# Performance work log

Hardware: AMD Instinct MI355X
Metric: run time of the kernel (lower is better)

The kernel has to match this reference:

```python
import jax, jax.numpy as jnp
import numpy as np

B, N, E, T, DIN, H, G, ND, NT, L = 4, 10000, 320000, 16, 16, 64, 64, 16, 3, 7


def _mlp2(x, W1, b1, W2, b2):
    # Linear -> LeakyReLU -> (Dropout: eval identity) -> Linear -> LeakyReLU
    h = jax.nn.leaky_relu(x @ W1 + b1)
    return jax.nn.leaky_relu(h @ W2 + b2)


def _gcn_conv(x, src, dst, ew, nt, W1, b1, W2, b2):
    # x: [B,N,D], nt: [B,N,ND], ew: [*,E,1] broadcastable over batch
    x_in = _mlp2(jnp.concatenate([x, nt], axis=-1), W1, b1, W2, b2)  # [B,N,G]
    msgs = x_in[:, src, :] * ew                                      # gather + weight, [B,E,G]
    aggr = jnp.zeros(x_in.shape, x_in.dtype).at[:, dst, :].add(msgs) # scatter-add, [B,N,G]
    return x + aggr


def _gru(x, Wx, Wh, bx, bh):
    # PyTorch-style GRU over time axis. x: [B,N,T,DIN] -> hs: [T,B,N,H]
    xw = jnp.einsum('bntd,dh->tbnh', x, Wx) + bx  # precompute input projections [T,B,N,3H]
    h0 = jnp.zeros(x.shape[:2] + (Wh.shape[0],), x.dtype)

    def step(h, xw_t):
        hw = h @ Wh + bh
        xr, xz, xn = jnp.split(xw_t, 3, axis=-1)
        hr, hz, hn = jnp.split(hw, 3, axis=-1)
        r = jax.nn.sigmoid(xr + hr)
        z = jax.nn.sigmoid(xz + hz)
        n = jnp.tanh(xn + r * hn)
        h_new = (1 - z) * n + z * h
        return h_new, h_new

    _, hs = jax.lax.scan(step, h0, xw)
    return hs


def reference(input_day, edge_attr, gru_Wx, gru_Wh, gru_bx, gru_bh,
              rnn_fc_W, rnn_fc_b,
              e_emb, e_c0_W1, e_c0_b1, e_c0_W2, e_c0_b2,
              e_c1_W1, e_c1_b1, e_c1_W2, e_c1_b2,
              e_fm_W1, e_fm_b1, e_fm_W2, e_fm_b2,
              g_emb, g_c0_W1, g_c0_b1, g_c0_W2, g_c0_b2,
              g_c1_W1, g_c1_b1, g_c1_W2, g_c1_b2,
              gcn_fc_W, gcn_fc_b,
              edge_index, node_type_ids):
    src, dst = edge_index[0], edge_index[1]

    # KRNN encoder (GRU) + max over time + FC head
    hs = _gru(input_day, gru_Wx, gru_Wh, gru_bx, gru_bh)  # [T,B,N,H]
    rnn_out = hs.max(axis=0)                              # kr_out.max(dim=-2) -> [B,N,H]
    y_rnn = rnn_out @ rnn_fc_W + rnn_fc_b                 # [B,N,L]

    # EdgeNet: GCN stack on static edge_attr, then per-edge pair MLP -> gate
    nt_e = jnp.broadcast_to(e_emb[node_type_ids][None], (B, N, ND))
    ew0 = edge_attr.reshape(1, E, 1)
    x = rnn_out
    x = _gcn_conv(x, src, dst, ew0, nt_e, e_c0_W1, e_c0_b1, e_c0_W2, e_c0_b2)
    x = _gcn_conv(x, src, dst, ew0, nt_e, e_c1_W1, e_c1_b1, e_c1_W2, e_c1_b2)
    edge_x = jnp.concatenate([x[:, src, :], x[:, dst, :]], axis=-1)  # [B,E,2G]
    h = jax.nn.leaky_relu(edge_x @ e_fm_W1 + e_fm_b1)
    edge_gate = jax.nn.relu(h @ e_fm_W2 + e_fm_b2)                   # [B,E,1]

    # Main GCNNet with learned edge gates
    nt_g = jnp.broadcast_to(g_emb[node_type_ids][None], (B, N, ND))
    x = rnn_out
    x = _gcn_conv(x, src, dst, edge_gate, nt_g, g_c0_W1, g_c0_b1, g_c0_W2, g_c0_b2)
    x = _gcn_conv(x, src, dst, edge_gate, nt_g, g_c1_W1, g_c1_b1, g_c1_W2, g_c1_b2)
    y_gcn = x @ gcn_fc_W + gcn_fc_b                                  # [B,N,L]

    return y_rnn + y_gcn


def setup_inputs() -> dict:
    key = jax.random.key(0)
    ks = iter(jax.random.split(key, 48))

    def nrm(shape, s=0.1):
        return jax.random.normal(next(ks), shape, jnp.float32) * s

    inp = {}
    inp['input_day'] = jax.random.normal(next(ks), (B, N, T, DIN), jnp.float32)
    inp['edge_index'] = jax.random.randint(next(ks), (2, E), 0, N)
    inp['node_type_ids'] = jax.random.randint(next(ks), (N,), 0, NT)
    inp['edge_attr'] = jax.random.uniform(next(ks), (E,), jnp.float32)

    inp['gru_Wx'] = nrm((DIN, 3 * H))
    inp['gru_Wh'] = nrm((H, 3 * H))
    inp['gru_bx'] = jnp.zeros((3 * H,), jnp.float32)
    inp['gru_bh'] = jnp.zeros((3 * H,), jnp.float32)
    inp['rnn_fc_W'] = nrm((H, L))
    inp['rnn_fc_b'] = jnp.zeros((L,), jnp.float32)

    inp['e_emb'] = nrm((NT, ND))
    inp['g_emb'] = nrm((NT, ND))
    for pre, in_dim in (('e_c0', H + ND), ('e_c1', G + ND), ('g_c0', H + ND), ('g_c1', G + ND)):
        inp[pre + '_W1'] = nrm((in_dim, G))
        inp[pre + '_b1'] = jnp.zeros((G,), jnp.float32)
        inp[pre + '_W2'] = nrm((G, G))
        inp[pre + '_b2'] = jnp.zeros((G,), jnp.float32)

    inp['e_fm_W1'] = nrm((2 * G, G))
    inp['e_fm_b1'] = jnp.zeros((G,), jnp.float32)
    inp['e_fm_W2'] = nrm((G, 1))
    inp['e_fm_b2'] = jnp.zeros((1,), jnp.float32)

    inp['gcn_fc_W'] = nrm((G, L))
    inp['gcn_fc_b'] = jnp.zeros((L,), jnp.float32)
    return inp
```

## Files before the change

### kernel.cpp

```cpp
#include <hip/hip_runtime.h>
#include <hip/hip_bf16.h>

#define NB 4
#define NN 10000
#define NE 320000
#define BN 40000
#define NL 7

typedef float f32x4 __attribute__((ext_vector_type(4)));
typedef __bf16 bf16x8 __attribute__((ext_vector_type(8)));

__device__ __forceinline__ float bf2f(unsigned short u){
  unsigned x = ((unsigned)u) << 16;
  return __builtin_bit_cast(float, x);
}
__device__ __forceinline__ unsigned short f2bf(float f){
  unsigned u = __builtin_bit_cast(unsigned, f);
  u += 0x7fffu + ((u >> 16) & 1u);
  return (unsigned short)(u >> 16);
}
__device__ __forceinline__ bf16x8 zero8(){
  uint4 z = make_uint4(0u,0u,0u,0u);
  return __builtin_bit_cast(bf16x8, z);
}
__device__ __forceinline__ bf16x8 one8(){
  uint4 z = make_uint4(0x3f80u,0u,0u,0u);
  return __builtin_bit_cast(bf16x8, z);
}
__device__ __forceinline__ bf16x8 ld8bf(const unsigned short* p){
  uint4 u = *(const uint4*)p;
  return __builtin_bit_cast(bf16x8, u);
}
__device__ __forceinline__ unsigned pk2(float lo, float hi){
  unsigned r;
  asm("v_cvt_pk_bf16_f32 %0, %1, %2" : "=v"(r) : "v"(lo), "v"(hi));
  return r;
}
__device__ __forceinline__ bf16x8 ld8f(const float* p){
  float4 a = *(const float4*)p;
  float4 b = *(const float4*)(p+4);
  uint4 u = make_uint4(pk2(a.x,a.y), pk2(a.z,a.w), pk2(b.x,b.y), pk2(b.z,b.w));
  return __builtin_bit_cast(bf16x8, u);
}
__device__ __forceinline__ float frcp(float x){ return __builtin_amdgcn_rcpf(x); }
__device__ __forceinline__ float tanh_(float x){ return 1.f - 2.f*frcp(__expf(2.f*x)+1.f); }
__device__ __forceinline__ float lrelu(float x){ return x > 0.f ? x : 0.01f*x; }

#define LDS_WAIT() asm volatile("s_waitcnt lgkmcnt(0)" ::: "memory")

__global__ __launch_bounds__(256, 2) void gru_kernel(
    const float* __restrict__ xd,
    const float* __restrict__ Wx,
    const float* __restrict__ Wh,
    const float* __restrict__ bx,
    const float* __restrict__ bh,
    float* __restrict__ rnn)
{
  __shared__ __attribute__((aligned(16))) unsigned short WhT[192][72];
  __shared__ __attribute__((aligned(16))) unsigned short WxT[192][40];
  __shared__ __attribute__((aligned(16))) unsigned short hb[4][16][76];
  int tid = threadIdx.x;
  int wave = tid >> 6, lane = tid & 63;
  int ln16 = lane & 15, quad = lane >> 4;

  for (int i = tid; i < 64*192; i += 256){
    int k = i / 192, n = i - k*192;
    WhT[n][k] = f2bf(Wh[i]);
  }
  for (int i = tid; i < 16*192; i += 256){
    int k = i / 192, n = i - k*192;
    WxT[n][k] = f2bf(Wx[i]);
    WxT[n][17+k] = 0;
  }
  if (tid < 192){
    float bias = (tid < 128) ? (bx[tid] + bh[tid]) : bx[tid];
    WxT[tid][16] = f2bf(bias);
  }
  for (int i = tid; i < 4*16*76; i += 256) ((unsigned short*)hb)[i] = 0;
  __syncthreads();

  int rowbase = blockIdx.x * 64 + wave * 16;

  bf16x8 whf[2][12];
  #pragma unroll
  for (int kt=0; kt<2; ++kt)
    #pragma unroll
    for (int nt=0; nt<12; ++nt)
      whf[kt][nt] = ld8bf(&WhT[nt*16 + ln16][kt*32 + quad*8]);

  f32x4 bhn2[4];
  #pragma unroll
  for (int j=0;j<4;++j)
    bhn2[j] = *(const f32x4*)(bh + 128 + j*16 + quad*4);

  f32x4 hprev[4], vmax[4];
  #pragma unroll
  for (int j=0;j<4;++j){
    hprev[j] = (f32x4){0.f,0.f,0.f,0.f};
    vmax[j]  = (f32x4){-1e30f,-1e30f,-1e30f,-1e30f};
  }

  const float* xrow = xd + (size_t)(rowbase + ln16) * 256;
  unsigned short* hrow = &hb[wave][ln16][0];

  bf16x8 axc;
  if (quad < 2) axc = ld8f(xrow + quad*8);
  else          axc = (quad == 2) ? one8() : zero8();

  for (int t = 0; t < 16; ++t){
    bf16x8 axn;
    if (quad < 2) axn = (t < 15) ? ld8f(xrow + (t+1)*16 + quad*8) : zero8();
    else          axn = (quad == 2) ? one8() : zero8();
    bf16x8 ah0 = ld8bf(hrow + quad*8);
    bf16x8 ah1 = ld8bf(hrow + 32 + quad*8);

    #pragma unroll
    for (int j=0;j<4;++j){
      bf16x8 xr = ld8bf(&WxT[j*16+ln16][quad*8]);
      bf16x8 xz = ld8bf(&WxT[(4+j)*16+ln16][quad*8]);
      bf16x8 xn = ld8bf(&WxT[(8+j)*16+ln16][quad*8]);
      f32x4 z4 = (f32x4){0.f,0.f,0.f,0.f};
      f32x4 ar = __builtin_amdgcn_mfma_f32_16x16x32_bf16(xr, axc, z4, 0,0,0);
      ar = __builtin_amdgcn_mfma_f32_16x16x32_bf16(whf[0][j], ah0, ar, 0,0,0);
      ar = __builtin_amdgcn_mfma_f32_16x16x32_bf16(whf[1][j], ah1, ar, 0,0,0);
      f32x4 az = __builtin_amdgcn_mfma_f32_16x16x32_bf16(xz, axc, z4, 0,0,0);
      az = __builtin_amdgcn_mfma_f32_16x16x32_bf16(whf[0][4+j], ah0, az, 0,0,0);
      az = __builtin_amdgcn_mfma_f32_16x16x32_bf16(whf[1][4+j], ah1, az, 0,0,0);
      f32x4 an = __builtin_amdgcn_mfma_f32_16x16x32_bf16(xn, axc, z4, 0,0,0);
      f32x4 ah = __builtin_amdgcn_mfma_f32_16x16x32_bf16(whf[0][8+j], ah0, bhn2[j], 0,0,0);
      ah = __builtin_amdgcn_mfma_f32_16x16x32_bf16(whf[1][8+j], ah1, ah, 0,0,0);
      f32x4 hv;
      #pragma unroll
      for (int i=0;i<4;++i){
        float Er = __expf(-ar[i]);
        float Ez = __expf(-az[i]);
        float pr = 1.f + Er, pz = 1.f + Ez;
        float D  = frcp(pr * pz);
        float r  = D * pz;
        float z  = D * pr;
        float nn = tanh_(an[i] + r * ah[i]);
        float h  = fmaf(z, hprev[j][i]-nn, nn);
        hprev[j][i] = h;
        vmax[j][i] = fmaxf(vmax[j][i], h);
        hv[i] = h;
      }
      *(uint2*)&hb[wave][ln16][j*16+quad*4] = make_uint2(pk2(hv[0],hv[1]), pk2(hv[2],hv[3]));
    }
    LDS_WAIT();
    axc = axn;
  }
  float* orow = rnn + (size_t)(rowbase + ln16)*64;
  #pragma unroll
  for (int j=0;j<4;++j)
    *(f32x4*)(orow + j*16 + quad*4) = vmax[j];
}

__global__ __launch_bounds__(256, 2) void mlp2_kernel(
    const float* __restrict__ x,
    const int* __restrict__ ntid,
    const float* __restrict__ emb,
    const float* __restrict__ W1,
    const float* __restrict__ b1,
    const float* __restrict__ W2,
    const float* __restrict__ b2,
    unsigned short* __restrict__ out)
{
  __shared__ __attribute__((aligned(16))) unsigned short W1T[64][96];
  __shared__ __attribute__((aligned(16))) unsigned short W2T[64][72];
  __shared__ __attribute__((aligned(16))) unsigned short hb[4][16][72];
  __shared__ float sb1[64], sb2[64];
  int tid = threadIdx.x;
  for (int i=tid;i<80*64;i+=256){ int k=i>>6, n=i&63; W1T[n][k]=f2bf(W1[i]); }
  for (int i=tid;i<64*16;i+=256){ int n=i>>4, k=80+(i&15); W1T[n][k]=0; }
  for (int i=tid;i<64*64;i+=256){ int k=i>>6, n=i&63; W2T[n][k]=f2bf(W2[i]); }
  if (tid<64){ sb1[tid]=b1[tid]; sb2[tid]=b2[tid]; }
  __syncthreads();

  int wave = tid>>6, lane = tid&63, ln16 = lane&15, quad = lane>>4;
  int row0 = blockIdx.x*64 + wave*16;
  int r_ = row0 + ln16;
  const float* xr = x + (size_t)r_*64;
  bf16x8 a0 = ld8f(xr + quad*8);
  bf16x8 a1 = ld8f(xr + 32 + quad*8);
  int id = ntid[r_ % NN];
  bf16x8 a2 = (quad<2) ? ld8f(emb + id*16 + quad*8) : zero8();

  f32x4 acc[4];
  #pragma unroll
  for (int nt=0;nt<4;++nt){
    float bb = sb1[nt*16+ln16];
    acc[nt] = (f32x4){bb,bb,bb,bb};
    acc[nt] = __builtin_amdgcn_mfma_f32_16x16x32_bf16(a0, ld8bf(&W1T[nt*16+ln16][quad*8]),    acc[nt], 0,0,0);
    acc[nt] = __builtin_amdgcn_mfma_f32_16x16x32_bf16(a1, ld8bf(&W1T[nt*16+ln16][32+quad*8]), acc[nt], 0,0,0);
    acc[nt] = __builtin_amdgcn_mfma_f32_16x16x32_bf16(a2, ld8bf(&W1T[nt*16+ln16][64+quad*8]), acc[nt], 0,0,0);
  }
  #pragma unroll
  for (int nt=0;nt<4;++nt)
    #pragma unroll
    for (int i=0;i<4;++i)
      hb[wave][quad*4+i][nt*16+ln16] = f2bf(lrelu(acc[nt][i]));
  LDS_WAIT();
  bf16x8 h0 = ld8bf(&hb[wave][ln16][quad*8]);
  bf16x8 h1 = ld8bf(&hb[wave][ln16][32+quad*8]);
  f32x4 acc2[4];
  #pragma unroll
  for (int nt=0;nt<4;++nt){
    float bb = sb2[nt*16+ln16];
    acc2[nt] = (f32x4){bb,bb,bb,bb};
    acc2[nt] = __builtin_amdgcn_mfma_f32_16x16x32_bf16(h0, ld8bf(&W2T[nt*16+ln16][quad*8]),    acc2[nt], 0,0,0);
    acc2[nt] = __builtin_amdgcn_mfma_f32_16x16x32_bf16(h1, ld8bf(&W2T[nt*16+ln16][32+quad*8]), acc2[nt], 0,0,0);
  }
  #pragma unroll
  for (int nt=0;nt<4;++nt)
    #pragma unroll
    for (int i=0;i<4;++i)
      out[(size_t)(row0+quad*4+i)*64 + nt*16+ln16] = f2bf(lrelu(acc2[nt][i]));
}

__global__ __launch_bounds__(256) void aggr_mlp_kernel(
    const float* __restrict__ x,
    const unsigned short* __restrict__ xin,
    const int* __restrict__ rowptr,
    const int* __restrict__ ssrc,
    const float* __restrict__ wp,
    int bstride,
    const int* __restrict__ ntid,
    const float* __restrict__ emb,
    const float* __restrict__ W1,
    const float* __restrict__ b1,
    const float* __restrict__ W2,
    const float* __restrict__ b2,
    float* __restrict__ xe_out,
    unsigned short* __restrict__ out)
{
  __shared__ __attribute__((aligned(16))) unsigned short W1T[64][96];
  __shared__ __attribute__((aligned(16))) unsigned short W2T[64][72];
  __shared__ __attribute__((aligned(16))) unsigned short hb[16][72];
  __shared__ __attribute__((aligned(16))) unsigned short h2[16][72];
  __shared__ float sb1[64], sb2[64];
  int tid = threadIdx.x;
  for (int i=tid;i<80*64;i+=256){ int k=i>>6, n=i&63; W1T[n][k]=f2bf(W1[i]); }
  for (int i=tid;i<64*16;i+=256){ int n=i>>4, k=80+(i&15); W1T[n][k]=0; }
  for (int i=tid;i<64*64;i+=256){ int k=i>>6, n=i&63; W2T[n][k]=f2bf(W2[i]); }
  if (tid<64){ sb1[tid]=b1[tid]; sb2[tid]=b2[tid]; }

  int wave = tid>>6, lane = tid&63, ln16 = lane&15, quad = lane>>4;
  int row0 = blockIdx.x*16;
  int b = row0 / NN;
  int r = wave*4 + quad;
  int row = row0 + r;
  int n = row - b*NN;
  int l = ln16;
  int p0 = rowptr[n], p1 = rowptr[n+1];
  const unsigned short* xb_ = xin + (size_t)b*NN*64;
  const float* wb = wp + (size_t)b*bstride;
  float a0=0.f, a1=0.f, a2=0.f, a3=0.f;
  #pragma unroll 4
  for (int p=p0; p<p1; ++p){
    int s = ssrc[p];
    float w = wb[p];
    uint2 m = *(const uint2*)(xb_ + (size_t)s*64 + l*4);
    a0 += bf2f((unsigned short)(m.x & 0xffffu)) * w;
    a1 += bf2f((unsigned short)(m.x >> 16)) * w;
    a2 += bf2f((unsigned short)(m.y & 0xffffu)) * w;
    a3 += bf2f((unsigned short)(m.y >> 16)) * w;
  }
  float4 base = *(const float4*)(x + (size_t)row*64 + l*4);
  float o0=base.x+a0, o1=base.y+a1, o2=base.z+a2, o3=base.w+a3;
  float4 ov; ov.x=o0; ov.y=o1; ov.z=o2; ov.w=o3;
  *(float4*)(xe_out + (size_t)row*64 + l*4) = ov;
  *(uint2*)&hb[r][l*4] = make_uint2(pk2(o0,o1), pk2(o2,o3));
  __syncthreads();

  int id = ntid[row0 + ln16 - b*NN];
  bf16x8 xa0 = ld8bf(&hb[ln16][quad*8]);
  bf16x8 xa1 = ld8bf(&hb[ln16][32+quad*8]);
  bf16x8 xa2 = (quad<2) ? ld8f(emb + id*16 + quad*8) : zero8();
  float bb = sb1[wave*16+ln16];
  f32x4 acc = (f32x4){bb,bb,bb,bb};
  acc = __builtin_amdgcn_mfma_f32_16x16x32_bf16(xa0, ld8bf(&W1T[wave*16+ln16][quad*8]),    acc, 0,0,0);
  acc = __builtin_amdgcn_mfma_f32_16x16x32_bf16(xa1, ld8bf(&W1T[wave*16+ln16][32+quad*8]), acc, 0,0,0);
  acc = __builtin_amdgcn_mfma_f32_16x16x32_bf16(xa2, ld8bf(&W1T[wave*16+ln16][64+quad*8]), acc, 0,0,0);
  #pragma unroll
  for (int i=0;i<4;++i)
    h2[quad*4+i][wave*16+ln16] = f2bf(lrelu(acc[i]));
  __syncthreads();
  bf16x8 hh0 = ld8bf(&h2[ln16][quad*8]);
  bf16x8 hh1 = ld8bf(&h2[ln16][32+quad*8]);
  float b2v = sb2[wave*16+ln16];
  f32x4 acc2 = (f32x4){b2v,b2v,b2v,b2v};
  acc2 = __builtin_amdgcn_mfma_f32_16x16x32_bf16(hh0, ld8bf(&W2T[wave*16+ln16][quad*8]),    acc2, 0,0,0);
  acc2 = __builtin_amdgcn_mfma_f32_16x16x32_bf16(hh1, ld8bf(&W2T[wave*16+ln16][32+quad*8]), acc2, 0,0,0);
  #pragma unroll
  for (int i=0;i<4;++i)
    out[(size_t)(row0+quad*4+i)*64 + wave*16+ln16] = f2bf(lrelu(acc2[i]));
}

__global__ __launch_bounds__(256) void aggr_uv_kernel(
    const float* __restrict__ x,
    const unsigned short* __restrict__ xin,
    const int* __restrict__ rowptr,
    const int* __restrict__ ssrc,
    const float* __restrict__ wp,
    int bstride,
    const float* __restrict__ W1,
    unsigned short* __restrict__ uvp)
{
  __shared__ __attribute__((aligned(16))) unsigned short WT[128][72];
  __shared__ __attribute__((aligned(16))) unsigned short hb[16][72];
  int tid = threadIdx.x;
  for (int i=tid;i<64*64;i+=256){
    int k=i>>6, n=i&63;
    WT[n][k]    = f2bf(W1[i]);
    WT[64+n][k] = f2bf(W1[64*64 + i]);
  }

  int wave = tid>>6, lane = tid&63, ln16 = lane&15, quad = lane>>4;
  int row0 = blockIdx.x*16;
  int b = row0 / NN;
  int r = wave*4 + quad;
  int row = row0 + r;
  int n = row - b*NN;
  int l = ln16;
  int p0 = rowptr[n], p1 = rowptr[n+1];
  const unsigned short* xb_ = xin + (size_t)b*NN*64;
  const float* wb = wp + (size_t)b*bstride;
  float a0=0.f, a1=0.f, a2=0.f, a3=0.f;
  #pragma unroll 4
  for (int p=p0; p<p1; ++p){
    int s = ssrc[p];
    float w = wb[p];
    uint2 m = *(const uint2*)(xb_ + (size_t)s*64 + l*4);
    a0 += bf2f((unsigned short)(m.x & 0xffffu)) * w;
    a1 += bf2f((unsigned short)(m.x >> 16)) * w;
    a2 += bf2f((unsigned short)(m.y & 0xffffu)) * w;
    a3 += bf2f((unsigned short)(m.y >> 16)) * w;
  }
  float4 base = *(const float4*)(x + (size_t)row*64 + l*4);
  float o0=base.x+a0, o1=base.y+a1, o2=base.z+a2, o3=base.w+a3;
  *(uint2*)&hb[r][l*4] = make_uint2(pk2(o0,o1), pk2(o2,o3));
  __syncthreads();

  bf16x8 xa0 = ld8bf(&hb[ln16][quad*8]);
  bf16x8 xa1 = ld8bf(&hb[ln16][32+quad*8]);
  #pragma unroll
  for (int t=0;t<2;++t){
    int nt = wave*2 + t;
    f32x4 acc = (f32x4){0.f,0.f,0.f,0.f};
    acc = __builtin_amdgcn_mfma_f32_16x16x32_bf16(xa0, ld8bf(&WT[nt*16+ln16][quad*8]),    acc, 0,0,0);
    acc = __builtin_amdgcn_mfma_f32_16x16x32_bf16(xa1, ld8bf(&WT[nt*16+ln16][32+quad*8]), acc, 0,0,0);
    #pragma unroll
    for (int i=0;i<4;++i)
      uvp[(size_t)(row0+quad*4+i)*128 + nt*16+ln16] = f2bf(acc[i]);
  }
}

__global__ __launch_bounds__(256) void count_kernel(const int* __restrict__ ei, int* __restrict__ counts){
  int e = blockIdx.x*256+threadIdx.x;
  atomicAdd(&counts[ei[NE+e]], 1);
}
__global__ __launch_bounds__(1024) void scan_kernel(const int* __restrict__ counts,
                                                    int* __restrict__ rowptr, int* __restrict__ cursor){
  __shared__ int incl[10240];
  __shared__ int wsum[16];
  int tid=threadIdx.x, wave=tid>>6, lane=tid&63;
  int base = wave*640;
  int carry=0;
  #pragma unroll
  for (int c=0;c<10;++c){
    int i = base + c*64 + lane;
    int v = (i<NN)? counts[i] : 0;
    int s = v;
    #pragma unroll
    for (int off=1;off<64;off<<=1){
      int t_ = __shfl_up(s, off);
      if (lane>=off) s += t_;
    }
    s += carry;
    incl[base + c*64 + lane] = s;
    carry = __shfl(s, 63);
  }
  if (lane==63) wsum[wave]=carry;
  __syncthreads();
  if (wave==0){
    int w_ = (lane<16)? wsum[lane]:0;
    #pragma unroll
    for (int off=1;off<16;off<<=1){
      int t_ = __shfl_up(w_, off);
      if (lane>=off) w_ += t_;
    }
    if (lane<16) wsum[lane]=w_;
  }
  __syncthreads();
  int woff = (wave>0)? wsum[wave-1] : 0;
  #pragma unroll
  for (int c=0;c<10;++c){
    int i = base + c*64 + lane;
    if (i<NN){
      int excl = incl[i] + woff - counts[i];
      rowptr[i]=excl; cursor[i]=excl;
    }
  }
  if (tid==0) rowptr[NN]=wsum[15];
}
__global__ __launch_bounds__(256) void fill_kernel(const int* __restrict__ ei,
                                                   const float* __restrict__ ea,
                                                   int* __restrict__ cursor,
                                                   int* __restrict__ ssrc,
                                                   float* __restrict__ wcsr){
  int e = blockIdx.x*256+threadIdx.x;
  int d = ei[NE+e];
  int pos = atomicAdd(&cursor[d],1);
  ssrc[pos]=ei[e];
  wcsr[pos]=ea[e];
}

__global__ __launch_bounds__(256) void aggr_final_kernel(
    const float* x,
    const unsigned short* __restrict__ xin,
    const int* __restrict__ rowptr,
    const int* __restrict__ ssrc,
    const float* __restrict__ wp,
    const float* __restrict__ rnn,
    const float* __restrict__ Wr, const float* __restrict__ br,
    const float* __restrict__ Wg, const float* __restrict__ bg,
    float* __restrict__ out)
{
  __shared__ float sWr[448], sWg[448], sb[7];
  int tid=threadIdx.x;
  for (int i=tid;i<448;i+=256){ sWr[i]=Wr[i]; sWg[i]=Wg[i]; }
  if (tid<7) sb[tid]=br[tid]+bg[tid];
  __syncthreads();
  int wave=tid>>6, lane=tid&63;
  int sub=lane>>4, l=lane&15;
  int bid = blockIdx.x*4 + wave;
  int b = bid / NN, n = bid - b*NN;
  int p0 = rowptr[n], p1 = rowptr[n+1];
  const unsigned short* xb_ = xin + (size_t)b*NN*64;
  const float* wb = wp + (size_t)b*NE;
  float a0=0.f, a1=0.f, a2=0.f, a3=0.f;
  #pragma unroll 4
  for (int p=p0+sub; p<p1; p+=4){
    int s = ssrc[p];
    float w = wb[p];
    uint2 m = *(const uint2*)(xb_ + (size_t)s*64 + l*4);
    a0 += bf2f((unsigned short)(m.x & 0xffffu)) * w;
    a1 += bf2f((unsigned short)(m.x >> 16)) * w;
    a2 += bf2f((unsigned short)(m.y & 0xffffu)) * w;
    a3 += bf2f((unsigned short)(m.y >> 16)) * w;
  }
  a0 += __shfl_xor(a0,16); a0 += __shfl_xor(a0,32);
  a1 += __shfl_xor(a1,16); a1 += __shfl_xor(a1,32);
  a2 += __shfl_xor(a2,16); a2 += __shfl_xor(a2,32);
  a3 += __shfl_xor(a3,16); a3 += __shfl_xor(a3,32);
  if (sub==0){
    float4 base = *(const float4*)(x + (size_t)bid*64 + l*4);
    float o0=base.x+a0, o1=base.y+a1, o2=base.z+a2, o3=base.w+a3;
    float4 rr = *(const float4*)(rnn + (size_t)bid*64 + l*4);
    float part[7];
    #pragma unroll
    for (int q=0;q<7;++q)
      part[q] = o0*sWg[(l*4+0)*7+q] + o1*sWg[(l*4+1)*7+q]
              + o2*sWg[(l*4+2)*7+q] + o3*sWg[(l*4+3)*7+q]
              + rr.x*sWr[(l*4+0)*7+q] + rr.y*sWr[(l*4+1)*7+q]
              + rr.z*sWr[(l*4+2)*7+q] + rr.w*sWr[(l*4+3)*7+q];
    #pragma unroll
    for (int q=0;q<7;++q){
      part[q] += __shfl_xor(part[q],1);
      part[q] += __shfl_xor(part[q],2);
      part[q] += __shfl_xor(part[q],4);
      part[q] += __shfl_xor(part[q],8);
    }
    if (l==0){
      #pragma unroll
      for (int q=0;q<7;++q) out[(size_t)bid*7+q] = part[q] + sb[q];
    }
  }
}

__global__ __launch_bounds__(256) void gate_kernel(
    const unsigned short* __restrict__ uvp,
    const int* __restrict__ rowptr,
    const int* __restrict__ ssrc,
    const float* __restrict__ b1,
    const float* __restrict__ W2,
    const float* __restrict__ b2,
    float* __restrict__ gate)
{
  int tid=threadIdx.x;
  int wave=tid>>6, lane=tid&63;
  int sub=lane>>4, l=lane&15;
  int bid = blockIdx.x*4 + wave;
  int b = bid / NN, n = bid - b*NN;
  int p0 = rowptr[n], p1 = rowptr[n+1];
  const unsigned short* ub = uvp + (size_t)b*NN*128;
  uint2 vu = *(const uint2*)(ub + (size_t)n*128 + 64 + l*4);
  float v0=bf2f((unsigned short)(vu.x&0xffffu)), v1=bf2f((unsigned short)(vu.x>>16));
  float v2=bf2f((unsigned short)(vu.y&0xffffu)), v3=bf2f((unsigned short)(vu.y>>16));
  float4 bb = *(const float4*)(b1 + l*4);
  float4 ww = *(const float4*)(W2 + l*4);
  float b2v = b2[0];
  float* gb = gate + (size_t)b*NE;
  #pragma unroll 4
  for (int p=p0+sub; p<p1; p+=4){
    int s = ssrc[p];
    uint2 uu = *(const uint2*)(ub + (size_t)s*128 + l*4);
    float h0 = lrelu(bf2f((unsigned short)(uu.x&0xffffu)) + v0 + bb.x);
    float h1 = lrelu(bf2f((unsigned short)(uu.x>>16))     + v1 + bb.y);
    float h2 = lrelu(bf2f((unsigned short)(uu.y&0xffffu)) + v2 + bb.z);
    float h3 = lrelu(bf2f((unsigned short)(uu.y>>16))     + v3 + bb.w);
    float part = h0*ww.x + h1*ww.y + h2*ww.z + h3*ww.w;
    part += __shfl_xor(part,1);
    part += __shfl_xor(part,2);
    part += __shfl_xor(part,4);
    part += __shfl_xor(part,8);
    if (l==0){
      float g = part + b2v;
      gb[p] = g>0.f ? g : 0.f;
    }
  }
}

extern "C" void kernel_launch(void* const* d_in, const int* in_sizes, int n_in,
                              void* d_out, int out_size, void* d_ws, size_t ws_size,
                              hipStream_t stream)
{
  (void)in_sizes; (void)n_in; (void)out_size; (void)ws_size;
  const float* input_day = (const float*)d_in[0];
  const int* ei    = (const int*)d_in[1];
  const int* ntid  = (const int*)d_in[2];
  const float* edge_attr = (const float*)d_in[3];
  const float* gWx = (const float*)d_in[4];
  const float* gWh = (const float*)d_in[5];
  const float* gbx = (const float*)d_in[6];
  const float* gbh = (const float*)d_in[7];
  const float* rW  = (const float*)d_in[8];
  const float* rb  = (const float*)d_in[9];
  const float* eemb= (const float*)d_in[10];
  const float* gemb= (const float*)d_in[11];
  const float* ec0W1=(const float*)d_in[12];
  const float* ec0b1=(const float*)d_in[13];
  const float* ec0W2=(const float*)d_in[14];
  const float* ec0b2=(const float*)d_in[15];
  const float* ec1W1=(const float*)d_in[16];
  const float* ec1b1=(const float*)d_in[17];
  const float* ec1W2=(const float*)d_in[18];
  const float* ec1b2=(const float*)d_in[19];
  const float* gc0W1=(const float*)d_in[20];
  const float* gc0b1=(const float*)d_in[21];
  const float* gc0W2=(const float*)d_in[22];
  const float* gc0b2=(const float*)d_in[23];
  const float* gc1W1=(const float*)d_in[24];
  const float* gc1b1=(const float*)d_in[25];
  const float* gc1W2=(const float*)d_in[26];
  const float* gc1b2=(const float*)d_in[27];
  const float* efmW1=(const float*)d_in[28];
  const float* efmb1=(const float*)d_in[29];
  const float* efmW2=(const float*)d_in[30];
  const float* efmb2=(const float*)d_in[31];
  const float* gcnW =(const float*)d_in[32];
  const float* gcnb =(const float*)d_in[33];

  char* ws = (char*)d_ws;
  float*          rnn = (float*)(ws);
  float*          xe  = (float*)(ws + 10240000);
  unsigned short* xinA= (unsigned short*)(ws + 20480000);
  unsigned short* uvp = (unsigned short*)(ws + 25600000);
  float*          gat = (float*)(ws + 35840000);
  int* rowptr= (int*)(ws + 40960000);
  int* cursor= (int*)(ws + 41000064);
  int* counts= (int*)(ws + 41040064);
  int*   ssrc= (int*)(ws + 41080064);
  float* wcsr= (float*)(ws + 42360064);
  unsigned short* xinB = (unsigned short*)gat;
  unsigned short* xinD = (unsigned short*)uvp;

  hipMemsetAsync(counts, 0, NN*sizeof(int), stream);
  count_kernel<<<NE/256, 256, 0, stream>>>(ei, counts);
  scan_kernel<<<1, 1024, 0, stream>>>(counts, rowptr, cursor);
  fill_kernel<<<NE/256, 256, 0, stream>>>(ei, edge_attr, cursor, ssrc, wcsr);

  gru_kernel<<<625, 256, 0, stream>>>(input_day, gWx, gWh, gbx, gbh, rnn);

  mlp2_kernel<<<625, 256, 0, stream>>>(rnn, ntid, eemb, ec0W1, ec0b1, ec0W2, ec0b2, xinA);
  aggr_mlp_kernel<<<BN/16, 256, 0, stream>>>(rnn, xinA, rowptr, ssrc, wcsr, 0,
                                             ntid, eemb, ec1W1, ec1b1, ec1W2, ec1b2,
                                             xe, xinB);
  aggr_uv_kernel<<<BN/16, 256, 0, stream>>>(xe, xinB, rowptr, ssrc, wcsr, 0,
                                            efmW1, uvp);
  gate_kernel<<<BN/4, 256, 0, stream>>>(uvp, rowptr, ssrc, efmb1, efmW2, efmb2, gat);

  mlp2_kernel<<<625, 256, 0, stream>>>(rnn, ntid, gemb, gc0W1, gc0b1, gc0W2, gc0b2, xinA);
  aggr_mlp_kernel<<<BN/16, 256, 0, stream>>>(rnn, xinA, rowptr, ssrc, gat, NE,
                                             ntid, gemb, gc1W1, gc1b1, gc1W2, gc1b2,
                                             xe, xinD);
  aggr_final_kernel<<<BN/4, 256, 0, stream>>>(xe, xinD, rowptr, ssrc, gat, rnn,
                                              rW, rb, gcnW, gcnb, (float*)d_out);
}
```

Measured before the change: 461.1 us.

## Horizontally fuse independent kernels into combined launches to cut launch count

Merges independent stages into shared launches that split on block index. The GRU now shares a launch with edge counting, the CSR fill with the first edge-net MLP, and the gate computation with the second GCN MLP. This removes three kernel launches and their boundaries, and lets small independent workloads overlap on the GPU. The cost is that every block of a merged kernel reserves the larger kernel's static LDS and register footprint. That can lower occupancy for the lightweight count, fill and gate blocks; the gate stage's gathers may suffer most.

```diff
diff --git a/kernel.cpp b/kernel.cpp
--- a/kernel.cpp
+++ b/kernel.cpp
@@ -48,14 +48,84 @@
 
 #define LDS_WAIT() asm volatile("s_waitcnt lgkmcnt(0)" ::: "memory")
 
-__global__ __launch_bounds__(256, 2) void gru_kernel(
+__device__ __forceinline__ void mlp2_body(
+    int bid,
+    const float* __restrict__ x,
+    const int* __restrict__ ntid,
+    const float* __restrict__ emb,
+    const float* __restrict__ W1,
+    const float* __restrict__ b1,
+    const float* __restrict__ W2,
+    const float* __restrict__ b2,
+    unsigned short* __restrict__ out)
+{
+  __shared__ __attribute__((aligned(16))) unsigned short W1T[64][96];
+  __shared__ __attribute__((aligned(16))) unsigned short W2T[64][72];
+  __shared__ __attribute__((aligned(16))) unsigned short hb[4][16][72];
+  __shared__ float sb1[64], sb2[64];
+  int tid = threadIdx.x;
+  for (int i=tid;i<80*64;i+=256){ int k=i>>6, n=i&63; W1T[n][k]=f2bf(W1[i]); }
+  for (int i=tid;i<64*16;i+=256){ int n=i>>4, k=80+(i&15); W1T[n][k]=0; }
+  for (int i=tid;i<64*64;i+=256){ int k=i>>6, n=i&63; W2T[n][k]=f2bf(W2[i]); }
+  if (tid<64){ sb1[tid]=b1[tid]; sb2[tid]=b2[tid]; }
+  __syncthreads();
+
+  int wave = tid>>6, lane = tid&63, ln16 = lane&15, quad = lane>>4;
+  int row0 = bid*64 + wave*16;
+  int r_ = row0 + ln16;
+  const float* xr = x + (size_t)r_*64;
+  bf16x8 a0 = ld8f(xr + quad*8);
+  bf16x8 a1 = ld8f(xr + 32 + quad*8);
+  int id = ntid[r_ % NN];
+  bf16x8 a2 = (quad<2) ? ld8f(emb + id*16 + quad*8) : zero8();
+
+  f32x4 acc[4];
+  #pragma unroll
+  for (int nt=0;nt<4;++nt){
+    float bb = sb1[nt*16+ln16];
+    acc[nt] = (f32x4){bb,bb,bb,bb};
+    acc[nt] = __builtin_amdgcn_mfma_f32_16x16x32_bf16(a0, ld8bf(&W1T[nt*16+ln16][quad*8]),    acc[nt], 0,0,0);
+    acc[nt] = __builtin_amdgcn_mfma_f32_16x16x32_bf16(a1, ld8bf(&W1T[nt*16+ln16][32+quad*8]), acc[nt], 0,0,0);
+    acc[nt] = __builtin_amdgcn_mfma_f32_16x16x32_bf16(a2, ld8bf(&W1T[nt*16+ln16][64+quad*8]), acc[nt], 0,0,0);
+  }
+  #pragma unroll
+  for (int nt=0;nt<4;++nt)
+    #pragma unroll
+    for (int i=0;i<4;++i)
+      hb[wave][quad*4+i][nt*16+ln16] = f2bf(lrelu(acc[nt][i]));
+  LDS_WAIT();
+  bf16x8 h0 = ld8bf(&hb[wave][ln16][quad*8]);
+  bf16x8 h1 = ld8bf(&hb[wave][ln16][32+quad*8]);
+  f32x4 acc2[4];
+  #pragma unroll
+  for (int nt=0;nt<4;++nt){
+    float bb = sb2[nt*16+ln16];
+    acc2[nt] = (f32x4){bb,bb,bb,bb};
+    acc2[nt] = __builtin_amdgcn_mfma_f32_16x16x32_bf16(h0, ld8bf(&W2T[nt*16+ln16][quad*8]),    acc2[nt], 0,0,0);
+    acc2[nt] = __builtin_amdgcn_mfma_f32_16x16x32_bf16(h1, ld8bf(&W2T[nt*16+ln16][32+quad*8]), acc2[nt], 0,0,0);
+  }
+  #pragma unroll
+  for (int nt=0;nt<4;++nt)
+    #pragma unroll
+    for (int i=0;i<4;++i)
+      out[(size_t)(row0+quad*4+i)*64 + nt*16+ln16] = f2bf(lrelu(acc2[nt][i]));
+}
+
+__global__ __launch_bounds__(256, 2) void gru_count_kernel(
     const float* __restrict__ xd,
     const float* __restrict__ Wx,
     const float* __restrict__ Wh,
     const float* __restrict__ bx,
     const float* __restrict__ bh,
-    float* __restrict__ rnn)
-{
+    float* __restrict__ rnn,
+    const int* __restrict__ ei,
+    int* __restrict__ counts)
+{
+  if (blockIdx.x >= 625){
+    int e = (blockIdx.x-625)*256 + threadIdx.x;
+    atomicAdd(&counts[ei[NE+e]], 1);
+    return;
+  }
   __shared__ __attribute__((aligned(16))) unsigned short WhT[192][72];
   __shared__ __attribute__((aligned(16))) unsigned short WxT[192][40];
   __shared__ __attribute__((aligned(16))) unsigned short hb[4][16][76];
@@ -155,66 +225,73 @@
     *(f32x4*)(orow + j*16 + quad*4) = vmax[j];
 }
 
-__global__ __launch_bounds__(256, 2) void mlp2_kernel(
+__global__ __launch_bounds__(1024) void scan_kernel(const int* __restrict__ counts,
+                                                    int* __restrict__ rowptr, int* __restrict__ cursor){
+  __shared__ int incl[10240];
+  __shared__ int wsum[16];
+  int tid=threadIdx.x, wave=tid>>6, lane=tid&63;
+  int base = wave*640;
+  int carry=0;
+  #pragma unroll
+  for (int c=0;c<10;++c){
+    int i = base + c*64 + lane;
+    int v = (i<NN)? counts[i] : 0;
+    int s = v;
+    #pragma unroll
+    for (int off=1;off<64;off<<=1){
+      int t_ = __shfl_up(s, off);
+      if (lane>=off) s += t_;
+    }
+    s += carry;
+    incl[base + c*64 + lane] = s;
+    carry = __shfl(s, 63);
+  }
+  if (lane==63) wsum[wave]=carry;
+  __syncthreads();
+  if (wave==0){
+    int w_ = (lane<16)? wsum[lane]:0;
+    #pragma unroll
+    for (int off=1;off<16;off<<=1){
+      int t_ = __shfl_up(w_, off);
+      if (lane>=off) w_ += t_;
+    }
+    if (lane<16) wsum[lane]=w_;
+  }
+  __syncthreads();
+  int woff = (wave>0)? wsum[wave-1] : 0;
+  #pragma unroll
+  for (int c=0;c<10;++c){
+    int i = base + c*64 + lane;
+    if (i<NN){
+      int excl = incl[i] + woff - counts[i];
+      rowptr[i]=excl; cursor[i]=excl;
+    }
+  }
+  if (tid==0) rowptr[NN]=wsum[15];
+}
+
+__global__ __launch_bounds__(256) void fill_mlp2e_kernel(
+    const int* __restrict__ ei,
+    const float* __restrict__ ea,
+    int* __restrict__ cursor,
+    int* __restrict__ ssrc,
+    float* __restrict__ wcsr,
     const float* __restrict__ x,
     const int* __restrict__ ntid,
     const float* __restrict__ emb,
-    const float* __restrict__ W1,
-    const float* __restrict__ b1,
-    const float* __restrict__ W2,
-    const float* __restrict__ b2,
+    const float* __restrict__ W1, const float* __restrict__ b1,
+    const float* __restrict__ W2, const float* __restrict__ b2,
     unsigned short* __restrict__ out)
 {
-  __shared__ __attribute__((aligned(16))) unsigned short W1T[64][96];
-  __shared__ __attribute__((aligned(16))) unsigned short W2T[64][72];
-  __shared__ __attribute__((aligned(16))) unsigned short hb[4][16][72];
-  __shared__ float sb1[64], sb2[64];
-  int tid = threadIdx.x;
-  for (int i=tid;i<80*64;i+=256){ int k=i>>6, n=i&63; W1T[n][k]=f2bf(W1[i]); }
-  for (int i=tid;i<64*16;i+=256){ int n=i>>4, k=80+(i&15); W1T[n][k]=0; }
-  for (int i=tid;i<64*64;i+=256){ int k=i>>6, n=i&63; W2T[n][k]=f2bf(W2[i]); }
-  if (tid<64){ sb1[tid]=b1[tid]; sb2[tid]=b2[tid]; }
-  __syncthreads();
-
-  int wave = tid>>6, lane = tid&63, ln16 = lane&15, quad = lane>>4;
-  int row0 = blockIdx.x*64 + wave*16;
-  int r_ = row0 + ln16;
-  const float* xr = x + (size_t)r_*64;
-  bf16x8 a0 = ld8f(xr + quad*8);
-  bf16x8 a1 = ld8f(xr + 32 + quad*8);
-  int id = ntid[r_ % NN];
-  bf16x8 a2 = (quad<2) ? ld8f(emb + id*16 + quad*8) : zero8();
-
-  f32x4 acc[4];
-  #pragma unroll
-  for (int nt=0;nt<4;++nt){
-    float bb = sb1[nt*16+ln16];
-    acc[nt] = (f32x4){bb,bb,bb,bb};
-    acc[nt] = __builtin_amdgcn_mfma_f32_16x16x32_bf16(a0, ld8bf(&W1T[nt*16+ln16][quad*8]),    acc[nt], 0,0,0);
-    acc[nt] = __builtin_amdgcn_mfma_f32_16x16x32_bf16(a1, ld8bf(&W1T[nt*16+ln16][32+quad*8]), acc[nt], 0,0,0);
-    acc[nt] = __builtin_amdgcn_mfma_f32_16x16x32_bf16(a2, ld8bf(&W1T[nt*16+ln16][64+quad*8]), acc[nt], 0,0,0);
-  }
-  #pragma unroll
-  for (int nt=0;nt<4;++nt)
-    #pragma unroll
-    for (int i=0;i<4;++i)
-      hb[wave][quad*4+i][nt*16+ln16] = f2bf(lrelu(acc[nt][i]));
-  LDS_WAIT();
-  bf16x8 h0 = ld8bf(&hb[wave][ln16][quad*8]);
-  bf16x8 h1 = ld8bf(&hb[wave][ln16][32+quad*8]);
-  f32x4 acc2[4];
-  #pragma unroll
-  for (int nt=0;nt<4;++nt){
-    float bb = sb2[nt*16+ln16];
-    acc2[nt] = (f32x4){bb,bb,bb,bb};
-    acc2[nt] = __builtin_amdgcn_mfma_f32_16x16x32_bf16(h0, ld8bf(&W2T[nt*16+ln16][quad*8]),    acc2[nt], 0,0,0);
-    acc2[nt] = __builtin_amdgcn_mfma_f32_16x16x32_bf16(h1, ld8bf(&W2T[nt*16+ln16][32+quad*8]), acc2[nt], 0,0,0);
-  }
-  #pragma unroll
-  for (int nt=0;nt<4;++nt)
-    #pragma unroll
-    for (int i=0;i<4;++i)
-      out[(size_t)(row0+quad*4+i)*64 + nt*16+ln16] = f2bf(lrelu(acc2[nt][i]));
+  if (blockIdx.x >= 625){
+    int e = (blockIdx.x-625)*256 + threadIdx.x;
+    int d = ei[NE+e];
+    int pos = atomicAdd(&cursor[d],1);
+    ssrc[pos]=ei[e];
+    wcsr[pos]=ea[e];
+    return;
+  }
+  mlp2_body(blockIdx.x, x, ntid, emb, W1, b1, W2, b2, out);
 }
 
 __global__ __launch_bounds__(256) void aggr_mlp_kernel(
@@ -355,142 +432,29 @@
   }
 }
 
-__global__ __launch_bounds__(256) void count_kernel(const int* __restrict__ ei, int* __restrict__ counts){
-  int e = blockIdx.x*256+threadIdx.x;
-  atomicAdd(&counts[ei[NE+e]], 1);
-}
-__global__ __launch_bounds__(1024) void scan_kernel(const int* __restrict__ counts,
-                                                    int* __restrict__ rowptr, int* __restrict__ cursor){
-  __shared__ int incl[10240];
-  __shared__ int wsum[16];
-  int tid=threadIdx.x, wave=tid>>6, lane=tid&63;
-  int base = wave*640;
-  int carry=0;
-  #pragma unroll
-  for (int c=0;c<10;++c){
-    int i = base + c*64 + lane;
-    int v = (i<NN)? counts[i] : 0;
-    int s = v;
-    #pragma unroll
-    for (int off=1;off<64;off<<=1){
-      int t_ = __shfl_up(s, off);
-      if (lane>=off) s += t_;
-    }
-    s += carry;
-    incl[base + c*64 + lane] = s;
-    carry = __shfl(s, 63);
-  }
-  if (lane==63) wsum[wave]=carry;
-  __syncthreads();
-  if (wave==0){
-    int w_ = (lane<16)? wsum[lane]:0;
-    #pragma unroll
-    for (int off=1;off<16;off<<=1){
-      int t_ = __shfl_up(w_, off);
-      if (lane>=off) w_ += t_;
-    }
-    if (lane<16) wsum[lane]=w_;
-  }
-  __syncthreads();
-  int woff = (wave>0)? wsum[wave-1] : 0;
-  #pragma unroll
-  for (int c=0;c<10;++c){
-    int i = base + c*64 + lane;
-    if (i<NN){
-      int excl = incl[i] + woff - counts[i];
-      rowptr[i]=excl; cursor[i]=excl;
-    }
-  }
-  if (tid==0) rowptr[NN]=wsum[15];
-}
-__global__ __launch_bounds__(256) void fill_kernel(const int* __restrict__ ei,
-                                                   const float* __restrict__ ea,
-                                                   int* __restrict__ cursor,
-                                                   int* __restrict__ ssrc,
-                                                   float* __restrict__ wcsr){
-  int e = blockIdx.x*256+threadIdx.x;
-  int d = ei[NE+e];
-  int pos = atomicAdd(&cursor[d],1);
-  ssrc[pos]=ei[e];
-  wcsr[pos]=ea[e];
-}
-
-__global__ __launch_bounds__(256) void aggr_final_kernel(
-    const float* x,
-    const unsigned short* __restrict__ xin,
-    const int* __restrict__ rowptr,
-    const int* __restrict__ ssrc,
-    const float* __restrict__ wp,
-    const float* __restrict__ rnn,
-    const float* __restrict__ Wr, const float* __restrict__ br,
-    const float* __restrict__ Wg, const float* __restrict__ bg,
-    float* __restrict__ out)
-{
-  __shared__ float sWr[448], sWg[448], sb[7];
-  int tid=threadIdx.x;
-  for (int i=tid;i<448;i+=256){ sWr[i]=Wr[i]; sWg[i]=Wg[i]; }
-  if (tid<7) sb[tid]=br[tid]+bg[tid];
-  __syncthreads();
-  int wave=tid>>6, lane=tid&63;
-  int sub=lane>>4, l=lane&15;
-  int bid = blockIdx.x*4 + wave;
-  int b = bid / NN, n = bid - b*NN;
-  int p0 = rowptr[n], p1 = rowptr[n+1];
-  const unsigned short* xb_ = xin + (size_t)b*NN*64;
-  const float* wb = wp + (size_t)b*NE;
-  float a0=0.f, a1=0.f, a2=0.f, a3=0.f;
-  #pragma unroll 4
-  for (int p=p0+sub; p<p1; p+=4){
-    int s = ssrc[p];
-    float w = wb[p];
-    uint2 m = *(const uint2*)(xb_ + (size_t)s*64 + l*4);
-    a0 += bf2f((unsigned short)(m.x & 0xffffu)) * w;
-    a1 += bf2f((unsigned short)(m.x >> 16)) * w;
-    a2 += bf2f((unsigned short)(m.y & 0xffffu)) * w;
-    a3 += bf2f((unsigned short)(m.y >> 16)) * w;
-  }
-  a0 += __shfl_xor(a0,16); a0 += __shfl_xor(a0,32);
-  a1 += __shfl_xor(a1,16); a1 += __shfl_xor(a1,32);
-  a2 += __shfl_xor(a2,16); a2 += __shfl_xor(a2,32);
-  a3 += __shfl_xor(a3,16); a3 += __shfl_xor(a3,32);
-  if (sub==0){
-    float4 base = *(const float4*)(x + (size_t)bid*64 + l*4);
-    float o0=base.x+a0, o1=base.y+a1, o2=base.z+a2, o3=base.w+a3;
-    float4 rr = *(const float4*)(rnn + (size_t)bid*64 + l*4);
-    float part[7];
-    #pragma unroll
-    for (int q=0;q<7;++q)
-      part[q] = o0*sWg[(l*4+0)*7+q] + o1*sWg[(l*4+1)*7+q]
-              + o2*sWg[(l*4+2)*7+q] + o3*sWg[(l*4+3)*7+q]
-              + rr.x*sWr[(l*4+0)*7+q] + rr.y*sWr[(l*4+1)*7+q]
-              + rr.z*sWr[(l*4+2)*7+q] + rr.w*sWr[(l*4+3)*7+q];
-    #pragma unroll
-    for (int q=0;q<7;++q){
-      part[q] += __shfl_xor(part[q],1);
-      part[q] += __shfl_xor(part[q],2);
-      part[q] += __shfl_xor(part[q],4);
-      part[q] += __shfl_xor(part[q],8);
-    }
-    if (l==0){
-      #pragma unroll
-      for (int q=0;q<7;++q) out[(size_t)bid*7+q] = part[q] + sb[q];
-    }
-  }
-}
-
-__global__ __launch_bounds__(256) void gate_kernel(
+__global__ __launch_bounds__(256) void gate_mlp2g_kernel(
     const unsigned short* __restrict__ uvp,
     const int* __restrict__ rowptr,
     const int* __restrict__ ssrc,
     const float* __restrict__ b1,
-    const float* __restrict__ W2,
+    const float* __restrict__ W2g,
     const float* __restrict__ b2,
-    float* __restrict__ gate)
-{
+    float* __restrict__ gate,
+    const float* __restrict__ x,
+    const int* __restrict__ ntid,
+    const float* __restrict__ emb,
+    const float* __restrict__ mW1, const float* __restrict__ mb1,
+    const float* __restrict__ mW2, const float* __restrict__ mb2,
+    unsigned short* __restrict__ mout)
+{
+  if (blockIdx.x < 625){
+    mlp2_body(blockIdx.x, x, ntid, emb, mW1, mb1, mW2, mb2, mout);
+    return;
+  }
   int tid=threadIdx.x;
   int wave=tid>>6, lane=tid&63;
   int sub=lane>>4, l=lane&15;
-  int bid = blockIdx.x*4 + wave;
+  int bid = (blockIdx.x-625)*4 + wave;
   int b = bid / NN, n = bid - b*NN;
   int p0 = rowptr[n], p1 = rowptr[n+1];
   const unsigned short* ub = uvp + (size_t)b*NN*128;
@@ -498,7 +462,7 @@
   float v0=bf2f((unsigned short)(vu.x&0xffffu)), v1=bf2f((unsigned short)(vu.x>>16));
   float v2=bf2f((unsigned short)(vu.y&0xffffu)), v3=bf2f((unsigned short)(vu.y>>16));
   float4 bb = *(const float4*)(b1 + l*4);
-  float4 ww = *(const float4*)(W2 + l*4);
+  float4 ww = *(const float4*)(W2g + l*4);
   float b2v = b2[0];
   float* gb = gate + (size_t)b*NE;
   #pragma unroll 4
@@ -517,6 +481,69 @@
     if (l==0){
       float g = part + b2v;
       gb[p] = g>0.f ? g : 0.f;
+    }
+  }
+}
+
+__global__ __launch_bounds__(256) void aggr_final_kernel(
+    const float* x,
+    const unsigned short* __restrict__ xin,
+    const int* __restrict__ rowptr,
+    const int* __restrict__ ssrc,
+    const float* __restrict__ wp,
+    const float* __restrict__ rnn,
+    const float* __restrict__ Wr, const float* __restrict__ br,
+    const float* __restrict__ Wg, const float* __restrict__ bg,
+    float* __restrict__ out)
+{
+  __shared__ float sWr[448], sWg[448], sb[7];
+  int tid=threadIdx.x;
+  for (int i=tid;i<448;i+=256){ sWr[i]=Wr[i]; sWg[i]=Wg[i]; }
+  if (tid<7) sb[tid]=br[tid]+bg[tid];
+  __syncthreads();
+  int wave=tid>>6, lane=tid&63;
+  int sub=lane>>4, l=lane&15;
+  int bid = blockIdx.x*4 + wave;
+  int b = bid / NN, n = bid - b*NN;
+  int p0 = rowptr[n], p1 = rowptr[n+1];
+  const unsigned short* xb_ = xin + (size_t)b*NN*64;
+  const float* wb = wp + (size_t)b*NE;
+  float a0=0.f, a1=0.f, a2=0.f, a3=0.f;
+  #pragma unroll 4
+  for (int p=p0+sub; p<p1; p+=4){
+    int s = ssrc[p];
+    float w = wb[p];
+    uint2 m = *(const uint2*)(xb_ + (size_t)s*64 + l*4);
+    a0 += bf2f((unsigned short)(m.x & 0xffffu)) * w;
+    a1 += bf2f((unsigned short)(m.x >> 16)) * w;
+    a2 += bf2f((unsigned short)(m.y & 0xffffu)) * w;
+    a3 += bf2f((unsigned short)(m.y >> 16)) * w;
+  }
+  a0 += __shfl_xor(a0,16); a0 += __shfl_xor(a0,32);
+  a1 += __shfl_xor(a1,16); a1 += __shfl_xor(a1,32);
+  a2 += __shfl_xor(a2,16); a2 += __shfl_xor(a2,32);
+  a3 += __shfl_xor(a3,16); a3 += __shfl_xor(a3,32);
+  if (sub==0){
+    float4 base = *(const float4*)(x + (size_t)bid*64 + l*4);
+    float o0=base.x+a0, o1=base.y+a1, o2=base.z+a2, o3=base.w+a3;
+    float4 rr = *(const float4*)(rnn + (size_t)bid*64 + l*4);
+    float part[7];
+    #pragma unroll
+    for (int q=0;q<7;++q)
+      part[q] = o0*sWg[(l*4+0)*7+q] + o1*sWg[(l*4+1)*7+q]
+              + o2*sWg[(l*4+2)*7+q] + o3*sWg[(l*4+3)*7+q]
+              + rr.x*sWr[(l*4+0)*7+q] + rr.y*sWr[(l*4+1)*7+q]
+              + rr.z*sWr[(l*4+2)*7+q] + rr.w*sWr[(l*4+3)*7+q];
+    #pragma unroll
+    for (int q=0;q<7;++q){
+      part[q] += __shfl_xor(part[q],1);
+      part[q] += __shfl_xor(part[q],2);
+      part[q] += __shfl_xor(part[q],4);
+      part[q] += __shfl_xor(part[q],8);
+    }
+    if (l==0){
+      #pragma unroll
+      for (int q=0;q<7;++q) out[(size_t)bid*7+q] = part[q] + sb[q];
     }
   }
 }
@@ -576,21 +603,21 @@
   unsigned short* xinD = (unsigned short*)uvp;
 
   hipMemsetAsync(counts, 0, NN*sizeof(int), stream);
-  count_kernel<<<NE/256, 256, 0, stream>>>(ei, counts);
+  gru_count_kernel<<<1875, 256, 0, stream>>>(input_day, gWx, gWh, gbx, gbh, rnn,
+                                             ei, counts);
   scan_kernel<<<1, 1024, 0, stream>>>(counts, rowptr, cursor);
-  fill_kernel<<<NE/256, 256, 0, stream>>>(ei, edge_attr, cursor, ssrc, wcsr);
-
-  gru_kernel<<<625, 256, 0, stream>>>(input_day, gWx, gWh, gbx, gbh, rnn);
-
-  mlp2_kernel<<<625, 256, 0, stream>>>(rnn, ntid, eemb, ec0W1, ec0b1, ec0W2, ec0b2, xinA);
+  fill_mlp2e_kernel<<<1875, 256, 0, stream>>>(ei, edge_attr, cursor, ssrc, wcsr,
+                                              rnn, ntid, eemb,
+                                              ec0W1, ec0b1, ec0W2, ec0b2, xinA);
   aggr_mlp_kernel<<<BN/16, 256, 0, stream>>>(rnn, xinA, rowptr, ssrc, wcsr, 0,
                                              ntid, eemb, ec1W1, ec1b1, ec1W2, ec1b2,
                                              xe, xinB);
   aggr_uv_kernel<<<BN/16, 256, 0, stream>>>(xe, xinB, rowptr, ssrc, wcsr, 0,
                                             efmW1, uvp);
-  gate_kernel<<<BN/4, 256, 0, stream>>>(uvp, rowptr, ssrc, efmb1, efmW2, efmb2, gat);
-
-  mlp2_kernel<<<625, 256, 0, stream>>>(rnn, ntid, gemb, gc0W1, gc0b1, gc0W2, gc0b2, xinA);
+  gate_mlp2g_kernel<<<10625, 256, 0, stream>>>(uvp, rowptr, ssrc,
+                                               efmb1, efmW2, efmb2, gat,
+                                               rnn, ntid, gemb,
+                                               gc0W1, gc0b1, gc0W2, gc0b2, xinA);
   aggr_mlp_kernel<<<BN/16, 256, 0, stream>>>(rnn, xinA, rowptr, ssrc, gat, NE,
                                              ntid, gemb, gc1W1, gc1b1, gc1W2, gc1b2,
                                              xe, xinD);
```

Result: no change. 453.8 us (-1.6%).
